# Kernel optimization log

Hardware: AMD Instinct MI355X
Metric: run time of the kernel (lower is better)

Reference implementation:

```python
import jax, jax.numpy as jnp
import numpy as np

N_NODES = 5000
N_EDGES = 40000
NUM_ATOM_TYPES = 100
HID = 32            # multiplicity of 0e and 1o in irreps_hidden
EDGE_ATTR_DIM = 8
NUM_BOND_TYPES = 5
OUT_SCALARS = 2 * 6 + 1  # max_charge=6 -> 13x0e
CUTOFF = 5.0
SQRT3 = 1.7320508075688772


def _sh(edge_vec):
    # o3.SphericalHarmonics('1x0e + 1x1o', normalize=True, normalization='component')
    d = jnp.sqrt(jnp.sum(edge_vec * edge_vec, axis=-1) + 1e-12)
    n = edge_vec / d[:, None]
    sh0 = jnp.ones(edge_vec.shape[0], edge_vec.dtype)          # [E]
    sh1 = SQRT3 * n[:, (1, 2, 0)]                              # [E,3], e3nn (y,z,x) order
    return sh0, sh1, d


def _soft_one_hot(d):
    # e3nn.math.soft_one_hot_linspace(d, 0, cutoff, 8, basis='gaussian', cutoff=True)
    values = jnp.linspace(0.0, CUTOFF, EDGE_ATTR_DIM + 2)[1:-1]
    step = CUTOFF / (EDGE_ATTR_DIM + 1)
    diff = (d[:, None] - values[None, :]) / step
    return jnp.exp(-diff * diff) / 1.12


def _mlp(x, W0, b0, W1, b1):
    # ScalarMLP(in, out, hidden=[in], SiLU)
    return jax.nn.silu(x @ W0 + b0) @ W1 + b1


def _tp_init(s, sh0, sh1, w):
    # FCTP(32x0e, 1x0e+1x1o -> 32x0e+32x1o); paths: 0e*0e->0e, 0e*1o->1o
    E = s.shape[0]
    w1 = w[:, : HID * HID].reshape(E, HID, HID)
    w2 = w[:, HID * HID :].reshape(E, HID, HID)
    c = 1.0 / np.sqrt(HID)  # fan-in = 32 per output irrep
    out_s = c * jnp.einsum('eu,euw->ew', s * sh0[:, None], w1)
    out_v = c * jnp.einsum('eu,ei,euw->ewi', s, sh1, w2)
    return out_s, out_v


def _tp_hidden(s, v, sh0, sh1, w):
    # FCTP(32x0e+32x1o, 1x0e+1x1o -> 32x0e+32x1o)
    # path order: 0e*0e->0e, 0e*1o->1o, 1o*0e->1o, 1o*1o->0e
    E = s.shape[0]
    ws = w.reshape(E, 4, HID, HID)
    c = 1.0 / np.sqrt(2 * HID)  # fan-in = 64 per output irrep
    dot = jnp.einsum('eui,ei->eu', v, sh1) / SQRT3  # CG(1,1->0) = delta/sqrt(3)
    out_s = c * (jnp.einsum('eu,euw->ew', s * sh0[:, None], ws[:, 0]) +
                 jnp.einsum('eu,euw->ew', dot, ws[:, 3]))
    out_v = c * (jnp.einsum('eu,ei,euw->ewi', s, sh1, ws[:, 1]) +
                 jnp.einsum('eui,euw->ewi', v * sh0[:, None, None], ws[:, 2]))
    return out_s, out_v


def _edge_tp(s1, v1, s2, v2, sh0, sh1, w):
    # FCTP(64x0e+64x1o (concat of two hidden), 1x0e+1x1o -> 5x0e)
    # blocks in concat order: s_src, v_src, s_dst, v_dst
    E = s1.shape[0]
    ws = w.reshape(E, 4, HID, NUM_BOND_TYPES)
    c = 1.0 / np.sqrt(4 * HID)  # fan-in = 128
    d1 = jnp.einsum('eui,ei->eu', v1, sh1) / SQRT3
    d2 = jnp.einsum('eui,ei->eu', v2, sh1) / SQRT3
    return c * (jnp.einsum('eu,euw->ew', s1 * sh0[:, None], ws[:, 0]) +
                jnp.einsum('eu,euw->ew', d1, ws[:, 1]) +
                jnp.einsum('eu,euw->ew', s2 * sh0[:, None], ws[:, 2]) +
                jnp.einsum('eu,euw->ew', d2, ws[:, 3]))


def _scatter_mean(ms, mv, dst, n):
    cnt = jax.ops.segment_sum(jnp.ones(dst.shape[0], ms.dtype), dst, num_segments=n)
    cnt = jnp.maximum(cnt, 1.0)
    s = jax.ops.segment_sum(ms, dst, num_segments=n) / cnt[:, None]
    v = jax.ops.segment_sum(mv, dst, num_segments=n) / cnt[:, None, None]
    return s, v


def setup_inputs() -> dict:
    key = jax.random.key(0)
    ks = jax.random.split(key, 16)
    def w(k, shape, fan_in):
        return jax.random.normal(k, shape, dtype=jnp.float32) / np.sqrt(fan_in)
    inp = {}
    inp['coordinates'] = jax.random.normal(ks[0], (N_NODES, 3), dtype=jnp.float32) * 1.5
    inp['atom_types'] = jax.random.randint(ks[1], (N_NODES,), 0, NUM_ATOM_TYPES)
    inp['edge_index'] = jax.random.randint(ks[2], (2, N_EDGES), 0, N_NODES)
    inp['atom_embed'] = jax.random.normal(ks[3], (NUM_ATOM_TYPES, HID), dtype=jnp.float32)
    inp['ip_W0'] = w(ks[4], (EDGE_ATTR_DIM, EDGE_ATTR_DIM), EDGE_ATTR_DIM)
    inp['ip_b0'] = jnp.zeros((EDGE_ATTR_DIM,), jnp.float32)
    inp['ip_W1'] = w(ks[5], (EDGE_ATTR_DIM, 2 * HID * HID), EDGE_ATTR_DIM)
    inp['ip_b1'] = jnp.zeros((2 * HID * HID,), jnp.float32)
    inp['ly_W0'] = w(ks[6], (EDGE_ATTR_DIM, EDGE_ATTR_DIM), EDGE_ATTR_DIM)
    inp['ly_b0'] = jnp.zeros((EDGE_ATTR_DIM,), jnp.float32)
    inp['ly_W1'] = w(ks[7], (EDGE_ATTR_DIM, 4 * HID * HID), EDGE_ATTR_DIM)
    inp['ly_b1'] = jnp.zeros((4 * HID * HID,), jnp.float32)
    inp['ly_Ws'] = jax.random.normal(ks[8], (HID, HID), dtype=jnp.float32)
    inp['ly_Wv'] = jax.random.normal(ks[9], (HID, HID), dtype=jnp.float32)
    inp['et_W0'] = w(ks[10], (EDGE_ATTR_DIM, EDGE_ATTR_DIM), EDGE_ATTR_DIM)
    inp['et_b0'] = jnp.zeros((EDGE_ATTR_DIM,), jnp.float32)
    inp['et_W1'] = w(ks[11], (EDGE_ATTR_DIM, 4 * HID * NUM_BOND_TYPES), EDGE_ATTR_DIM)
    inp['et_b1'] = jnp.zeros((4 * HID * NUM_BOND_TYPES,), jnp.float32)
    inp['no_W1'] = jax.random.normal(ks[12], (HID, OUT_SCALARS), dtype=jnp.float32)
    inp['no_W2'] = jax.random.normal(ks[13], (OUT_SCALARS, OUT_SCALARS), dtype=jnp.float32)
    return inp


def reference(coordinates, atom_types, edge_index, atom_embed,
              ip_W0, ip_b0, ip_W1, ip_b1,
              ly_W0, ly_b0, ly_W1, ly_b1, ly_Ws, ly_Wv,
              et_W0, et_b0, et_W1, et_b1, no_W1, no_W2):
    n = coordinates.shape[0]
    src, dst = edge_index[0], edge_index[1]
    edge_vec = coordinates[dst] - coordinates[src]
    sh0, sh1, d = _sh(edge_vec)
    edge_attr = _soft_one_hot(d)                              # [E,8]
    # initial projector: Conv(32x0e -> 32x0e+32x1o)
    s0 = atom_embed[atom_types]                               # [N,32]
    w_ip = _mlp(edge_attr, ip_W0, ip_b0, ip_W1, ip_b1)        # [E,2048]
    ms, mv = _tp_init(s0[src], sh0, sh1, w_ip)
    s, v = _scatter_mean(ms, mv, dst, n)                      # [N,32],[N,32,3]
    # one LinearSelfInteraction(Conv) layer
    w_ly = _mlp(edge_attr, ly_W0, ly_b0, ly_W1, ly_b1)        # [E,4096]
    ms, mv = _tp_hidden(s[src], v[src], sh0, sh1, w_ly)
    cs, cv = _scatter_mean(ms, mv, dst, n)
    lc = 1.0 / np.sqrt(HID)  # e3nn o3.Linear normalization
    s = cs + lc * (s @ ly_Ws)
    v = cv + lc * jnp.einsum('eui,uw->ewi', v, ly_Wv)
    # edge output: FCTP([h_src, h_dst], edge_sh) with radial weights
    w_et = _mlp(edge_attr, et_W0, et_b0, et_W1, et_b1)        # [E,640]
    edge_out = _edge_tp(s[src], v[src], s[dst], v[dst], sh0, sh1, w_et)  # [E,5]
    # node output MLP on detached scalar channel (13x0e)
    sd = jax.lax.stop_gradient(s)
    h = jax.nn.silu(sd @ no_W1 / np.sqrt(HID))
    node_out = h @ no_W2 / np.sqrt(OUT_SCALARS)               # [N,13]
    return edge_out, node_out
```

## Files before the change

### kernel.cpp

```cpp
#include <hip/hip_runtime.h>

#define NN 5000
#define NE 40000
#define HB 320

typedef unsigned int u32;
typedef unsigned short u16;
typedef __fp16 h16x2 __attribute__((ext_vector_type(2)));
typedef _Float16 f16x8 __attribute__((ext_vector_type(8)));
typedef __attribute__((ext_vector_type(4))) float f32x4;

union AF { u32 u[4]; f16x8 v; uint4 q; };

__device__ __forceinline__ float siluf(float x) { return x / (1.f + __expf(-x)); }

__device__ __forceinline__ u32 f2bf_u(float f) {
  u32 x = __float_as_uint(f);
  return (x + 0x7FFFu + ((x >> 16) & 1u)) >> 16;
}
__device__ __forceinline__ u16 f2bf(float f) { return (u16)f2bf_u(f); }
__device__ __forceinline__ float bf2f(u16 v) { return __uint_as_float(((u32)v) << 16); }
__device__ __forceinline__ u32 packbf2(float lo, float hi) {
  return f2bf_u(lo) | (f2bf_u(hi) << 16);
}
__device__ __forceinline__ u32 pkh2(float a, float b) {
  union { h16x2 h; u32 u; } r;
  r.h = __builtin_amdgcn_cvt_pkrtz(a, b);
  return r.u;
}
__device__ __forceinline__ u16 f2h(float v) {
  _Float16 h = (_Float16)v;
  return *(u16*)&h;
}
__device__ __forceinline__ void unpack8(uint4 q, float* f) {
  f[0] = __uint_as_float(q.x << 16); f[1] = __uint_as_float(q.x & 0xFFFF0000u);
  f[2] = __uint_as_float(q.y << 16); f[3] = __uint_as_float(q.y & 0xFFFF0000u);
  f[4] = __uint_as_float(q.z << 16); f[5] = __uint_as_float(q.z & 0xFFFF0000u);
  f[6] = __uint_as_float(q.w << 16); f[7] = __uint_as_float(q.w & 0xFFFF0000u);
}
__device__ __forceinline__ float dot8f(const float* h, const float* w, float init) {
  float a = init;
#pragma unroll
  for (int k = 0; k < 8; k++) a = fmaf(h[k], w[k], a);
  return a;
}
__device__ __forceinline__ void mlp8(const float* ea, const float* __restrict__ W0,
                                     const float* __restrict__ b0, float* h) {
#pragma unroll
  for (int j = 0; j < 8; j++) {
    float a = b0[j];
#pragma unroll
    for (int i = 0; i < 8; i++) a += ea[i] * W0[i*8 + j];
    h[j] = siluf(a);
  }
}
__device__ __forceinline__ AF mkfrag(float hs, const float* s) {
  AF a;
  a.u[0] = pkh2(hs*s[0], hs*s[1]);
  a.u[1] = pkh2(hs*s[2], hs*s[3]);
  a.u[2] = pkh2(hs*s[4], hs*s[5]);
  a.u[3] = pkh2(hs*s[6], hs*s[7]);
  return a;
}

__global__ __launch_bounds__(256) void k_conv1g(
    const float* __restrict__ coords, const int* __restrict__ eidx,
    const float* __restrict__ emb, const int* __restrict__ atype,
    const float* __restrict__ ipW0, const float* __restrict__ ipb0,
    const float* __restrict__ lyW0, const float* __restrict__ lyb0,
    const float* __restrict__ etW0, const float* __restrict__ etb0,
    const float* __restrict__ W1, const float* __restrict__ b1,
    const float* __restrict__ lyW1, const float* __restrict__ lyb1,
    float* __restrict__ sh, float* __restrict__ h_ip,
    float* __restrict__ h_ly, float* __restrict__ h_et,
    int* __restrict__ cur, int* __restrict__ perm,
    u16* __restrict__ msg, u16* __restrict__ lyT) {
  if (blockIdx.x >= HB) {
    int b = blockIdx.x - HB;
    int h = b >> 3;
    int t0 = (b & 7)*2304 + threadIdx.x*9;
#pragma unroll
    for (int j = 0; j < 9; j++) {
      int t = t0 + j;
      int kch = t >> 9, rem = t & 511;
      int col = rem >> 3, kk = rem & 7;
      int k = kch*8 + kk;
      int basec = (h == 0) ? ((col >> 5)*1024 + (col & 31))
                           : ((col < 32) ? (2048 + col) : (3072 + (col - 32)));
      float v = (k < 256) ? lyW1[(k >> 5)*4096 + basec + (k & 31)*32]
                          : lyb1[basec + (k - 256)*32];
      lyT[h*18432 + t] = f2h(v);
    }
    return;
  }
  __shared__ __align__(16) u16 B2[36*64*8];
  {
    int col = threadIdx.x & 63, pth = col >> 5, w = col & 31;
    int k0 = (threadIdx.x >> 6) * 72;
    for (int k = k0; k < k0 + 72; k++) {
      float v = (k < 256) ? W1[(k >> 5)*2048 + pth*1024 + (k & 31)*32 + w]
                          : b1[pth*1024 + (k - 256)*32 + w];
      B2[((k >> 3)*64 + col)*8 + (k & 7)] = f2h(v);
    }
  }
  if (threadIdx.x < 128) {
    int idx = threadIdx.x;
    int w = (idx >> 4) & 3, j = idx >> 6, m = idx & 15;
    int tile = blockIdx.x*4 + w + j*(HB*4);
    if (tile*16 < NE) {
      int e = tile*16 + m;
      int s = eidx[e], d = eidx[NE + e];
      float vx = coords[d*3+0] - coords[s*3+0];
      float vy = coords[d*3+1] - coords[s*3+1];
      float vz = coords[d*3+2] - coords[s*3+2];
      float dist = sqrtf(vx*vx + vy*vy + vz*vz + 1e-12f);
      float inv = 1.f / dist;
      const float SQ3 = 1.7320508075688772f;
      sh[e*3+0] = SQ3 * vy * inv;
      sh[e*3+1] = SQ3 * vz * inv;
      sh[e*3+2] = SQ3 * vx * inv;
      float ea[8];
      const float step = 5.f / 9.f;
#pragma unroll
      for (int jj = 0; jj < 8; jj++) {
        float diff = (dist - step * (float)(jj+1)) * (9.f / 5.f);
        ea[jj] = __expf(-diff*diff) * (1.f / 1.12f);
      }
      float h[8];
      mlp8(ea, ipW0, ipb0, h);
#pragma unroll
      for (int jj = 0; jj < 8; jj++) h_ip[e*8+jj] = h[jj];
      mlp8(ea, lyW0, lyb0, h);
#pragma unroll
      for (int jj = 0; jj < 8; jj++) h_ly[e*8+jj] = h[jj];
      mlp8(ea, etW0, etb0, h);
#pragma unroll
      for (int jj = 0; jj < 8; jj++) h_et[e*8+jj] = h[jj];
      int* cp = &cur[d];
      atomicCAS(cp, (int)0xAAAAAAAA, 0);
      int t = atomicAdd(cp, 1);
      if (t < 64) perm[d*64 + t] = e;
    }
  }
  __syncthreads();
  int lane = threadIdx.x & 63;
  int m = lane & 15, q = lane >> 4, wid = threadIdx.x >> 6;
  const float cs = 0.17677669529663687f;
  for (int tile = blockIdx.x*4 + wid; tile*16 < NE; tile += HB*4) {
    int e = tile*16 + m;
    int srow = atype[eidx[e]];
    float4 sA = *(const float4*)&emb[srow*32 + q*8];
    float4 sB = *(const float4*)&emb[srow*32 + q*8 + 4];
    float4 hA = *(const float4*)&h_ip[e*8];
    float4 hB = *(const float4*)&h_ip[e*8 + 4];
    float sf[8] = {sA.x,sA.y,sA.z,sA.w,sB.x,sB.y,sB.z,sB.w};
    float hf[8] = {hA.x,hA.y,hA.z,hA.w,hB.x,hB.y,hB.z,hB.w};
    f32x4 acc0 = {0.f,0.f,0.f,0.f}, acc1 = acc0, acc2 = acc0, acc3 = acc0;
#pragma unroll
    for (int ks = 0; ks < 9; ks++) {
      float hs = (ks < 8) ? hf[ks] : 1.f;
      AF a = mkfrag(hs, sf);
      int c2 = (ks*4 + q)*64;
      AF b0, b1f, b2, b3;
      b0.q  = *(const uint4*)&B2[(c2 +  0 + m)*8];
      b1f.q = *(const uint4*)&B2[(c2 + 16 + m)*8];
      b2.q  = *(const uint4*)&B2[(c2 + 32 + m)*8];
      b3.q  = *(const uint4*)&B2[(c2 + 48 + m)*8];
      acc0 = __builtin_amdgcn_mfma_f32_16x16x32_f16(a.v, b0.v,  acc0, 0, 0, 0);
      acc1 = __builtin_amdgcn_mfma_f32_16x16x32_f16(a.v, b1f.v, acc1, 0, 0, 0);
      acc2 = __builtin_amdgcn_mfma_f32_16x16x32_f16(a.v, b2.v,  acc2, 0, 0, 0);
      acc3 = __builtin_amdgcn_mfma_f32_16x16x32_f16(a.v, b3.v,  acc3, 0, 0, 0);
    }
#pragma unroll
    for (int r = 0; r < 4; r++) {
      int et = tile*16 + q*4 + r;
      u16* mp = msg + (size_t)et*128;
      mp[m]      = f2bf(cs*acc0[r]);
      mp[16 + m] = f2bf(cs*acc1[r]);
      float s0v = sh[et*3+0], s1v = sh[et*3+1], s2v = sh[et*3+2];
      float m0 = cs*acc2[r], m1 = cs*acc3[r];
      mp[32 +      m] = f2bf(m0*s0v);
      mp[64 +      m] = f2bf(m0*s1v);
      mp[96 +      m] = f2bf(m0*s2v);
      mp[32 + 16 + m] = f2bf(m1*s0v);
      mp[64 + 16 + m] = f2bf(m1*s1v);
      mp[96 + 16 + m] = f2bf(m1*s2v);
    }
  }
}

__global__ __launch_bounds__(256) void k_conv2(
    const float* __restrict__ hE, const float* __restrict__ sh,
    const float* __restrict__ s1, const float* __restrict__ v1soa,
    const int* __restrict__ eidx, const u16* __restrict__ lyT,
    u16* __restrict__ msgA, u16* __restrict__ msgB) {
  __shared__ __align__(16) u16 B2[36*64*8];
  const bool scalarHalf = blockIdx.x < HB;
  int blk = scalarHalf ? blockIdx.x : blockIdx.x - HB;
  {
    const uint4* src4 = (const uint4*)(lyT + (scalarHalf ? 0 : 18432));
    uint4* dst4 = (uint4*)B2;
    for (int t = threadIdx.x; t < 2304; t += 256) dst4[t] = src4[t];
  }
  __syncthreads();
  int lane = threadIdx.x & 63;
  int m = lane & 15, q = lane >> 4, wid = threadIdx.x >> 6;
  const float c = 0.125f;
  for (int tile = blk*4 + wid; tile*16 < NE; tile += HB*4) {
    int e = tile*16 + m;
    int srcn = eidx[e];
    float4 hA = *(const float4*)&hE[e*8];
    float4 hB = *(const float4*)&hE[e*8 + 4];
    float hf[8] = {hA.x,hA.y,hA.z,hA.w,hB.x,hB.y,hB.z,hB.w};

    if (scalarHalf) {
      float4 sA = *(const float4*)&s1[srcn*32 + q*8];
      float4 sB = *(const float4*)&s1[srcn*32 + q*8 + 4];
      float sf[8] = {sA.x,sA.y,sA.z,sA.w,sB.x,sB.y,sB.z,sB.w};
      f32x4 acc0 = {0.f,0.f,0.f,0.f}, acc1 = acc0, acc2 = acc0, acc3 = acc0;
#pragma unroll
      for (int ks = 0; ks < 9; ks++) {
        float hs = (ks < 8) ? hf[ks] : 1.f;
        AF a = mkfrag(hs, sf);
        int c2 = (ks*4 + q)*64;
        AF b0, b1f, b2, b3;
        b0.q  = *(const uint4*)&B2[(c2 +  0 + m)*8];
        b1f.q = *(const uint4*)&B2[(c2 + 16 + m)*8];
        b2.q  = *(const uint4*)&B2[(c2 + 32 + m)*8];
        b3.q  = *(const uint4*)&B2[(c2 + 48 + m)*8];
        acc0 = __builtin_amdgcn_mfma_f32_16x16x32_f16(a.v, b0.v,  acc0, 0, 0, 0);
        acc1 = __builtin_amdgcn_mfma_f32_16x16x32_f16(a.v, b1f.v, acc1, 0, 0, 0);
        acc2 = __builtin_amdgcn_mfma_f32_16x16x32_f16(a.v, b2.v,  acc2, 0, 0, 0);
        acc3 = __builtin_amdgcn_mfma_f32_16x16x32_f16(a.v, b3.v,  acc3, 0, 0, 0);
      }
#pragma unroll
      for (int r = 0; r < 4; r++) {
        int et = tile*16 + q*4 + r;
        u16* mp = msgA + (size_t)et*128;
        mp[m]      = f2bf(c*acc0[r]);
        mp[16 + m] = f2bf(c*acc1[r]);
        float s0v = sh[et*3+0], s1v = sh[et*3+1], s2v = sh[et*3+2];
        float m0 = c*acc2[r], m1 = c*acc3[r];
        mp[32 +      m] = f2bf(m0*s0v);
        mp[64 +      m] = f2bf(m0*s1v);
        mp[96 +      m] = f2bf(m0*s2v);
        mp[32 + 16 + m] = f2bf(m1*s0v);
        mp[64 + 16 + m] = f2bf(m1*s1v);
        mp[96 + 16 + m] = f2bf(m1*s2v);
      }
    } else {
      const float is3 = 0.5773502691896258f;
      float vf[3][8];
#pragma unroll
      for (int i = 0; i < 3; i++) {
        float4 aa = *(const float4*)&v1soa[i*160000 + srcn*32 + q*8];
        float4 bb = *(const float4*)&v1soa[i*160000 + srcn*32 + q*8 + 4];
        vf[i][0]=aa.x; vf[i][1]=aa.y; vf[i][2]=aa.z; vf[i][3]=aa.w;
        vf[i][4]=bb.x; vf[i][5]=bb.y; vf[i][6]=bb.z; vf[i][7]=bb.w;
      }
      float es0 = sh[e*3+0], es1 = sh[e*3+1], es2 = sh[e*3+2];
      float df[8];
#pragma unroll
      for (int j = 0; j < 8; j++)
        df[j] = (vf[0][j]*es0 + vf[1][j]*es1 + vf[2][j]*es2) * is3;
      f32x4 z = {0.f,0.f,0.f,0.f};
      f32x4 aV00 = z, aV01 = z, aV10 = z, aV11 = z, aV20 = z, aV21 = z, aD0 = z, aD1 = z;
#pragma unroll
      for (int ks = 0; ks < 9; ks++) {
        float hs = (ks < 8) ? hf[ks] : 1.f;
        int c2 = (ks*4 + q)*64;
        AF b0, b1f, b2, b3;
        b0.q  = *(const uint4*)&B2[(c2 +  0 + m)*8];
        b1f.q = *(const uint4*)&B2[(c2 + 16 + m)*8];
        b2.q  = *(const uint4*)&B2[(c2 + 32 + m)*8];
        b3.q  = *(const uint4*)&B2[(c2 + 48 + m)*8];
        AF a0 = mkfrag(hs, vf[0]);
        AF a1 = mkfrag(hs, vf[1]);
        AF a2 = mkfrag(hs, vf[2]);
        AF ad = mkfrag(hs, df);
        aV00 = __builtin_amdgcn_mfma_f32_16x16x32_f16(a0.v, b0.v,  aV00, 0, 0, 0);
        aV01 = __builtin_amdgcn_mfma_f32_16x16x32_f16(a0.v, b1f.v, aV01, 0, 0, 0);
        aV10 = __builtin_amdgcn_mfma_f32_16x16x32_f16(a1.v, b0.v,  aV10, 0, 0, 0);
        aV11 = __builtin_amdgcn_mfma_f32_16x16x32_f16(a1.v, b1f.v, aV11, 0, 0, 0);
        aV20 = __builtin_amdgcn_mfma_f32_16x16x32_f16(a2.v, b0.v,  aV20, 0, 0, 0);
        aV21 = __builtin_amdgcn_mfma_f32_16x16x32_f16(a2.v, b1f.v, aV21, 0, 0, 0);
        aD0  = __builtin_amdgcn_mfma_f32_16x16x32_f16(ad.v, b2.v,  aD0,  0, 0, 0);
        aD1  = __builtin_amdgcn_mfma_f32_16x16x32_f16(ad.v, b3.v,  aD1,  0, 0, 0);
      }
#pragma unroll
      for (int r = 0; r < 4; r++) {
        int et = tile*16 + q*4 + r;
        u16* mp = msgB + (size_t)et*128;
        mp[m]      = f2bf(c*aD0[r]);
        mp[16 + m] = f2bf(c*aD1[r]);
        mp[32 +      m] = f2bf(c*aV00[r]);
        mp[32 + 16 + m] = f2bf(c*aV01[r]);
        mp[64 +      m] = f2bf(c*aV10[r]);
        mp[64 + 16 + m] = f2bf(c*aV11[r]);
        mp[96 +      m] = f2bf(c*aV20[r]);
        mp[96 + 16 + m] = f2bf(c*aV21[r]);
      }
    }
  }
}

__global__ __launch_bounds__(256) void k_gather1(
    const u16* __restrict__ msg, const int* __restrict__ perm,
    const int* __restrict__ cur, float* __restrict__ s1,
    float* __restrict__ v1soa) {
  __shared__ int pe[2][64];
  int ln = threadIdx.x >> 7, c = threadIdx.x & 127;
  int n = blockIdx.x*2 + ln;
  int deg = min(cur[n], 64);
  if (c < 64) pe[ln][c] = perm[n*64 + c];
  __syncthreads();
  float acc = 0.f;
  for (int j = 0; j < deg; j++)
    acc += bf2f(msg[(size_t)pe[ln][j]*128 + c]);
  acc /= (float)max(deg, 1);
  if (c < 32) s1[n*32 + c] = acc;
  else { int i = (c-32) >> 5, w = (c-32) & 31; v1soa[i*160000 + n*32 + w] = acc; }
}

__global__ __launch_bounds__(256) void k_gather2(
    const u16* __restrict__ msgA, const u16* __restrict__ msgB,
    const int* __restrict__ perm, const int* __restrict__ cur,
    const float* __restrict__ s1, const float* __restrict__ v1soa,
    const float* __restrict__ Ws, const float* __restrict__ Wv,
    const float* __restrict__ noW1, const float* __restrict__ noW2,
    float* __restrict__ s2, float* __restrict__ v2, float* __restrict__ outN) {
  __shared__ int pe[2][64];
  __shared__ float sb[2][32];
  __shared__ float hb[2][13];
  int ln = threadIdx.x >> 7, c = threadIdx.x & 127;
  int n = blockIdx.x*2 + ln;
  int deg = min(cur[n], 64);
  if (c < 64) pe[ln][c] = perm[n*64 + c];
  __syncthreads();
  float acc = 0.f;
  for (int j = 0; j < deg; j++) {
    int e = pe[ln][j];
    acc += bf2f(msgA[(size_t)e*128 + c]) + bf2f(msgB[(size_t)e*128 + c]);
  }
  acc /= (float)max(deg, 1);
  const float lc = 0.17677669529663687f;
  if (c < 32) {
    float ss = 0.f;
#pragma unroll 8
    for (int u = 0; u < 32; u++) ss += s1[n*32 + u] * Ws[u*32 + c];
    float val = acc + lc*ss;
    s2[n*32 + c] = val;
    sb[ln][c] = val;
  } else {
    int i = (c-32) >> 5, w = (c-32) & 31;
    float sv = 0.f;
#pragma unroll 8
    for (int u = 0; u < 32; u++) sv += v1soa[i*160000 + n*32 + u] * Wv[u*32 + w];
    v2[n*96 + w*3 + i] = acc + lc*sv;
  }
  __syncthreads();
  const float i32 = 0.17677669529663687f;
  if (c < 13) {
    float a = 0.f;
#pragma unroll 8
    for (int u = 0; u < 32; u++) a += sb[ln][u] * noW1[u*13 + c];
    hb[ln][c] = siluf(a * i32);
  }
  __syncthreads();
  const float i13 = 0.2773500981126146f;
  if (c < 13) {
    float a = 0.f;
#pragma unroll
    for (int j = 0; j < 13; j++) a += hb[ln][j] * noW2[j*13 + c];
    outN[n*13 + c] = a * i13;
  }
}

__global__ __launch_bounds__(256) void k_e3(
    const float* __restrict__ hE, const float* __restrict__ sh,
    const float* __restrict__ s2, const float* __restrict__ v2,
    const int* __restrict__ eidx,
    const float* __restrict__ W1, const float* __restrict__ b1,
    float* __restrict__ out) {
  __shared__ uint4 WQ[640];
  __shared__ float BQ[640];
  for (int t = threadIdx.x; t < 640; t += 256) {
    int u = t & 31, pw = t >> 5, p2 = pw / 5, w = pw - p2*5;
    int col = p2*160 + u*5 + w;
    const float* s = W1 + col;
    uint4 q;
    q.x = packbf2(s[0],      s[640]);
    q.y = packbf2(s[1280],   s[1920]);
    q.z = packbf2(s[2560],   s[3200]);
    q.w = packbf2(s[3840],   s[4480]);
    WQ[t] = q;
    BQ[t] = b1[col];
  }
  __syncthreads();
  const int g = threadIdx.x >> 5, tw = threadIdx.x & 31;
  const float c = 0.08838834764831845f;
  const float is3 = 0.5773502691896258f;
  for (int p = blockIdx.x*8 + g; p*2 < NE; p += gridDim.x*8) {
    int e0 = p*2, e1 = e0 + 1;
    float h0[8], h1[8];
    {
      float4 qa = *(const float4*)&hE[e0*8];
      float4 qb = *(const float4*)&hE[e0*8+4];
      h0[0]=qa.x; h0[1]=qa.y; h0[2]=qa.z; h0[3]=qa.w;
      h0[4]=qb.x; h0[5]=qb.y; h0[6]=qb.z; h0[7]=qb.w;
      float4 qc = *(const float4*)&hE[e1*8];
      float4 qd = *(const float4*)&hE[e1*8+4];
      h1[0]=qc.x; h1[1]=qc.y; h1[2]=qc.z; h1[3]=qc.w;
      h1[4]=qd.x; h1[5]=qd.y; h1[6]=qd.z; h1[7]=qd.w;
    }
    int sA = eidx[e0], dA = eidx[NE+e0];
    int sB = eidx[e1], dB = eidx[NE+e1];
    float sa0 = sh[e0*3+0], sa1 = sh[e0*3+1], sa2 = sh[e0*3+2];
    float sb0 = sh[e1*3+0], sb1 = sh[e1*3+1], sb2 = sh[e1*3+2];
    float c00 = s2[sA*32 + tw];
    float c01 = (v2[sA*96+tw*3+0]*sa0 + v2[sA*96+tw*3+1]*sa1 + v2[sA*96+tw*3+2]*sa2) * is3;
    float c02 = s2[dA*32 + tw];
    float c03 = (v2[dA*96+tw*3+0]*sa0 + v2[dA*96+tw*3+1]*sa1 + v2[dA*96+tw*3+2]*sa2) * is3;
    float c10 = s2[sB*32 + tw];
    float c11 = (v2[sB*96+tw*3+0]*sb0 + v2[sB*96+tw*3+1]*sb1 + v2[sB*96+tw*3+2]*sb2) * is3;
    float c12 = s2[dB*32 + tw];
    float c13 = (v2[dB*96+tw*3+0]*sb0 + v2[dB*96+tw*3+1]*sb1 + v2[dB*96+tw*3+2]*sb2) * is3;
    float part0[5] = {0,0,0,0,0};
    float part1[5] = {0,0,0,0,0};
#pragma unroll
    for (int pp = 0; pp < 4; pp++) {
      float cp0 = (pp==0) ? c00 : (pp==1) ? c01 : (pp==2) ? c02 : c03;
      float cp1 = (pp==0) ? c10 : (pp==1) ? c11 : (pp==2) ? c12 : c13;
#pragma unroll
      for (int w = 0; w < 5; w++) {
        int idx = (pp*5 + w)*32 + tw;
        float f[8];
        unpack8(WQ[idx], f);
        float bv = BQ[idx];
        part0[w] = fmaf(cp0, dot8f(h0, f, bv), part0[w]);
        part1[w] = fmaf(cp1, dot8f(h1, f, bv), part1[w]);
      }
    }
#pragma unroll
    for (int off = 16; off > 0; off >>= 1)
#pragma unroll
      for (int w = 0; w < 5; w++) {
        part0[w] += __shfl_xor(part0[w], off, 32);
        part1[w] += __shfl_xor(part1[w], off, 32);
      }
    float outv = 0.f;
#pragma unroll
    for (int w = 0; w < 5; w++) {
      if (tw == w)     outv = part0[w];
      if (tw == 5 + w) outv = part1[w];
    }
    if (tw < 10) out[e0*5 + tw] = c * outv;
  }
}

extern "C" void kernel_launch(void* const* d_in, const int* in_sizes, int n_in,
                              void* d_out, int out_size, void* d_ws, size_t ws_size,
                              hipStream_t stream) {
  (void)in_sizes; (void)n_in; (void)out_size; (void)ws_size;
  const float* coords = (const float*)d_in[0];
  const int*   atype  = (const int*)d_in[1];
  const int*   eidx   = (const int*)d_in[2];
  const float* emb    = (const float*)d_in[3];
  const float* ipW0 = (const float*)d_in[4];
  const float* ipb0 = (const float*)d_in[5];
  const float* ipW1 = (const float*)d_in[6];
  const float* ipb1 = (const float*)d_in[7];
  const float* lyW0 = (const float*)d_in[8];
  const float* lyb0 = (const float*)d_in[9];
  const float* lyW1 = (const float*)d_in[10];
  const float* lyb1 = (const float*)d_in[11];
  const float* lyWs = (const float*)d_in[12];
  const float* lyWv = (const float*)d_in[13];
  const float* etW0 = (const float*)d_in[14];
  const float* etb0 = (const float*)d_in[15];
  const float* etW1 = (const float*)d_in[16];
  const float* etb1 = (const float*)d_in[17];
  const float* noW1 = (const float*)d_in[18];
  const float* noW2 = (const float*)d_in[19];

  float* ws = (float*)d_ws;
  float* sh    = ws;
  float* h_ip  = ws + 120000;
  float* h_ly  = ws + 440000;
  float* h_et  = ws + 760000;
  float* s1    = ws + 1240000;
  float* v1soa = ws + 1400000;
  float* s2    = ws + 1880000;
  float* v2    = ws + 2040000;
  int*   cur   = (int*)(ws + 2520000);
  int*   perm  = (int*)(ws + 2525000);
  u16*   msgA  = (u16*)(ws + 2845000);
  u16*   msgB  = (u16*)(ws + 5405000);
  u16*   lyT   = (u16*)(ws + 7965000);

  float* outE = (float*)d_out;
  float* outN = (float*)d_out + NE*5;

  k_conv1g<<<HB + 16, 256, 0, stream>>>(coords, eidx, emb, atype,
                                        ipW0, ipb0, lyW0, lyb0, etW0, etb0,
                                        ipW1, ipb1, lyW1, lyb1,
                                        sh, h_ip, h_ly, h_et, cur, perm, msgA, lyT);
  k_gather1<<<NN/2, 256, 0, stream>>>(msgA, perm, cur, s1, v1soa);
  k_conv2<<<2*HB, 256, 0, stream>>>(h_ly, sh, s1, v1soa, eidx, lyT, msgA, msgB);
  k_gather2<<<NN/2, 256, 0, stream>>>(msgA, msgB, perm, cur, s1, v1soa,
                                      lyWs, lyWv, noW1, noW2, s2, v2, outN);
  k_e3<<<1024, 256, 0, stream>>>(h_et, sh, s2, v2, eidx, etW1, etb1, outE);
}
```

Baseline: 170.0 us.

## Use one tile-group per block, keep per-edge data in LDS, unroll gathers

Raises the block count so each block handles exactly four 16-edge tiles (625*64 = 40000), which removes the grid-stride loops in conv1 and conv2. The per-edge radial hidden values, spherical harmonics and source atom types now stay in shared memory instead of going through the h_ip global buffer, and the h_ly/h_et stores become float4. The gather kernels unroll the neighbour sum by four to get more loads in flight, and k_e3 gets more blocks. In exchange, every block re-converts the full W1 weight tile into LDS, so that setup work is repeated across about twice as many blocks.

```diff
diff --git a/kernel.cpp b/kernel.cpp
--- a/kernel.cpp
+++ b/kernel.cpp
@@ -2,7 +2,7 @@
 
 #define NN 5000
 #define NE 40000
-#define HB 320
+#define HB 625
 
 typedef unsigned int u32;
 typedef unsigned short u16;
@@ -71,8 +71,7 @@
     const float* __restrict__ etW0, const float* __restrict__ etb0,
     const float* __restrict__ W1, const float* __restrict__ b1,
     const float* __restrict__ lyW1, const float* __restrict__ lyb1,
-    float* __restrict__ sh, float* __restrict__ h_ip,
-    float* __restrict__ h_ly, float* __restrict__ h_et,
+    float* __restrict__ sh, float* __restrict__ h_ly, float* __restrict__ h_et,
     int* __restrict__ cur, int* __restrict__ perm,
     u16* __restrict__ msg, u16* __restrict__ lyT) {
   if (blockIdx.x >= HB) {
@@ -94,6 +93,9 @@
     return;
   }
   __shared__ __align__(16) u16 B2[36*64*8];
+  __shared__ float hl[64][9];
+  __shared__ float shl[64][4];
+  __shared__ int   sAl[64];
   {
     int col = threadIdx.x & 63, pth = col >> 5, w = col & 31;
     int k0 = (threadIdx.x >> 6) * 72;
@@ -103,58 +105,60 @@
       B2[((k >> 3)*64 + col)*8 + (k & 7)] = f2h(v);
     }
   }
-  if (threadIdx.x < 128) {
+  if (threadIdx.x < 64) {
     int idx = threadIdx.x;
-    int w = (idx >> 4) & 3, j = idx >> 6, m = idx & 15;
-    int tile = blockIdx.x*4 + w + j*(HB*4);
-    if (tile*16 < NE) {
-      int e = tile*16 + m;
-      int s = eidx[e], d = eidx[NE + e];
-      float vx = coords[d*3+0] - coords[s*3+0];
-      float vy = coords[d*3+1] - coords[s*3+1];
-      float vz = coords[d*3+2] - coords[s*3+2];
-      float dist = sqrtf(vx*vx + vy*vy + vz*vz + 1e-12f);
-      float inv = 1.f / dist;
-      const float SQ3 = 1.7320508075688772f;
-      sh[e*3+0] = SQ3 * vy * inv;
-      sh[e*3+1] = SQ3 * vz * inv;
-      sh[e*3+2] = SQ3 * vx * inv;
-      float ea[8];
-      const float step = 5.f / 9.f;
-#pragma unroll
-      for (int jj = 0; jj < 8; jj++) {
-        float diff = (dist - step * (float)(jj+1)) * (9.f / 5.f);
-        ea[jj] = __expf(-diff*diff) * (1.f / 1.12f);
-      }
-      float h[8];
-      mlp8(ea, ipW0, ipb0, h);
-#pragma unroll
-      for (int jj = 0; jj < 8; jj++) h_ip[e*8+jj] = h[jj];
-      mlp8(ea, lyW0, lyb0, h);
-#pragma unroll
-      for (int jj = 0; jj < 8; jj++) h_ly[e*8+jj] = h[jj];
-      mlp8(ea, etW0, etb0, h);
-#pragma unroll
-      for (int jj = 0; jj < 8; jj++) h_et[e*8+jj] = h[jj];
-      int* cp = &cur[d];
-      atomicCAS(cp, (int)0xAAAAAAAA, 0);
-      int t = atomicAdd(cp, 1);
-      if (t < 64) perm[d*64 + t] = e;
-    }
+    int w = (idx >> 4) & 3, m = idx & 15;
+    int tile = blockIdx.x*4 + w;
+    int e = tile*16 + m;
+    int s = eidx[e], d = eidx[NE + e];
+    float vx = coords[d*3+0] - coords[s*3+0];
+    float vy = coords[d*3+1] - coords[s*3+1];
+    float vz = coords[d*3+2] - coords[s*3+2];
+    float dist = sqrtf(vx*vx + vy*vy + vz*vz + 1e-12f);
+    float inv = 1.f / dist;
+    const float SQ3 = 1.7320508075688772f;
+    float s0 = SQ3 * vy * inv;
+    float s1 = SQ3 * vz * inv;
+    float s2 = SQ3 * vx * inv;
+    sh[e*3+0] = s0; sh[e*3+1] = s1; sh[e*3+2] = s2;
+    shl[idx][0] = s0; shl[idx][1] = s1; shl[idx][2] = s2;
+    sAl[idx] = atype[s];
+    float ea[8];
+    const float step = 5.f / 9.f;
+#pragma unroll
+    for (int jj = 0; jj < 8; jj++) {
+      float diff = (dist - step * (float)(jj+1)) * (9.f / 5.f);
+      ea[jj] = __expf(-diff*diff) * (1.f / 1.12f);
+    }
+    float h[8];
+    mlp8(ea, ipW0, ipb0, h);
+#pragma unroll
+    for (int jj = 0; jj < 8; jj++) hl[idx][jj] = h[jj];
+    mlp8(ea, lyW0, lyb0, h);
+    { float4 f0 = {h[0],h[1],h[2],h[3]}, f1 = {h[4],h[5],h[6],h[7]};
+      *(float4*)&h_ly[e*8] = f0; *(float4*)&h_ly[e*8+4] = f1; }
+    mlp8(ea, etW0, etb0, h);
+    { float4 f0 = {h[0],h[1],h[2],h[3]}, f1 = {h[4],h[5],h[6],h[7]};
+      *(float4*)&h_et[e*8] = f0; *(float4*)&h_et[e*8+4] = f1; }
+    int* cp = &cur[d];
+    atomicCAS(cp, (int)0xAAAAAAAA, 0);
+    int t = atomicAdd(cp, 1);
+    if (t < 64) perm[d*64 + t] = e;
   }
   __syncthreads();
   int lane = threadIdx.x & 63;
   int m = lane & 15, q = lane >> 4, wid = threadIdx.x >> 6;
   const float cs = 0.17677669529663687f;
-  for (int tile = blockIdx.x*4 + wid; tile*16 < NE; tile += HB*4) {
-    int e = tile*16 + m;
-    int srow = atype[eidx[e]];
+  int tile = blockIdx.x*4 + wid;
+  {
+    int le = wid*16 + m;
+    int srow = sAl[le];
     float4 sA = *(const float4*)&emb[srow*32 + q*8];
     float4 sB = *(const float4*)&emb[srow*32 + q*8 + 4];
-    float4 hA = *(const float4*)&h_ip[e*8];
-    float4 hB = *(const float4*)&h_ip[e*8 + 4];
     float sf[8] = {sA.x,sA.y,sA.z,sA.w,sB.x,sB.y,sB.z,sB.w};
-    float hf[8] = {hA.x,hA.y,hA.z,hA.w,hB.x,hB.y,hB.z,hB.w};
+    float hf[8];
+#pragma unroll
+    for (int k = 0; k < 8; k++) hf[k] = hl[le][k];
     f32x4 acc0 = {0.f,0.f,0.f,0.f}, acc1 = acc0, acc2 = acc0, acc3 = acc0;
 #pragma unroll
     for (int ks = 0; ks < 9; ks++) {
@@ -173,11 +177,12 @@
     }
 #pragma unroll
     for (int r = 0; r < 4; r++) {
+      int lr = wid*16 + q*4 + r;
       int et = tile*16 + q*4 + r;
       u16* mp = msg + (size_t)et*128;
       mp[m]      = f2bf(cs*acc0[r]);
       mp[16 + m] = f2bf(cs*acc1[r]);
-      float s0v = sh[et*3+0], s1v = sh[et*3+1], s2v = sh[et*3+2];
+      float s0v = shl[lr][0], s1v = shl[lr][1], s2v = shl[lr][2];
       float m0 = cs*acc2[r], m1 = cs*acc3[r];
       mp[32 +      m] = f2bf(m0*s0v);
       mp[64 +      m] = f2bf(m0*s1v);
@@ -206,7 +211,8 @@
   int lane = threadIdx.x & 63;
   int m = lane & 15, q = lane >> 4, wid = threadIdx.x >> 6;
   const float c = 0.125f;
-  for (int tile = blk*4 + wid; tile*16 < NE; tile += HB*4) {
+  int tile = blk*4 + wid;
+  {
     int e = tile*16 + m;
     int srcn = eidx[e];
     float4 hA = *(const float4*)&hE[e*8];
@@ -315,7 +321,16 @@
   if (c < 64) pe[ln][c] = perm[n*64 + c];
   __syncthreads();
   float acc = 0.f;
-  for (int j = 0; j < deg; j++)
+  int j = 0;
+  for (; j + 4 <= deg; j += 4) {
+    int e0 = pe[ln][j], e1 = pe[ln][j+1], e2 = pe[ln][j+2], e3 = pe[ln][j+3];
+    float x0 = bf2f(msg[(size_t)e0*128 + c]);
+    float x1 = bf2f(msg[(size_t)e1*128 + c]);
+    float x2 = bf2f(msg[(size_t)e2*128 + c]);
+    float x3 = bf2f(msg[(size_t)e3*128 + c]);
+    acc += (x0 + x1) + (x2 + x3);
+  }
+  for (; j < deg; j++)
     acc += bf2f(msg[(size_t)pe[ln][j]*128 + c]);
   acc /= (float)max(deg, 1);
   if (c < 32) s1[n*32 + c] = acc;
@@ -338,7 +353,16 @@
   if (c < 64) pe[ln][c] = perm[n*64 + c];
   __syncthreads();
   float acc = 0.f;
-  for (int j = 0; j < deg; j++) {
+  int j = 0;
+  for (; j + 4 <= deg; j += 4) {
+    int e0 = pe[ln][j], e1 = pe[ln][j+1], e2 = pe[ln][j+2], e3 = pe[ln][j+3];
+    float x0 = bf2f(msgA[(size_t)e0*128 + c]) + bf2f(msgB[(size_t)e0*128 + c]);
+    float x1 = bf2f(msgA[(size_t)e1*128 + c]) + bf2f(msgB[(size_t)e1*128 + c]);
+    float x2 = bf2f(msgA[(size_t)e2*128 + c]) + bf2f(msgB[(size_t)e2*128 + c]);
+    float x3 = bf2f(msgA[(size_t)e3*128 + c]) + bf2f(msgB[(size_t)e3*128 + c]);
+    acc += (x0 + x1) + (x2 + x3);
+  }
+  for (; j < deg; j++) {
     int e = pe[ln][j];
     acc += bf2f(msgA[(size_t)e*128 + c]) + bf2f(msgB[(size_t)e*128 + c]);
   }
@@ -371,7 +395,7 @@
   if (c < 13) {
     float a = 0.f;
 #pragma unroll
-    for (int j = 0; j < 13; j++) a += hb[ln][j] * noW2[j*13 + c];
+    for (int j2 = 0; j2 < 13; j2++) a += hb[ln][j2] * noW2[j2*13 + c];
     outN[n*13 + c] = a * i13;
   }
 }
@@ -485,7 +509,6 @@
 
   float* ws = (float*)d_ws;
   float* sh    = ws;
-  float* h_ip  = ws + 120000;
   float* h_ly  = ws + 440000;
   float* h_et  = ws + 760000;
   float* s1    = ws + 1240000;
@@ -504,10 +527,10 @@
   k_conv1g<<<HB + 16, 256, 0, stream>>>(coords, eidx, emb, atype,
                                         ipW0, ipb0, lyW0, lyb0, etW0, etb0,
                                         ipW1, ipb1, lyW1, lyb1,
-                                        sh, h_ip, h_ly, h_et, cur, perm, msgA, lyT);
+                                        sh, h_ly, h_et, cur, perm, msgA, lyT);
   k_gather1<<<NN/2, 256, 0, stream>>>(msgA, perm, cur, s1, v1soa);
   k_conv2<<<2*HB, 256, 0, stream>>>(h_ly, sh, s1, v1soa, eidx, lyT, msgA, msgB);
   k_gather2<<<NN/2, 256, 0, stream>>>(msgA, msgB, perm, cur, s1, v1soa,
                                       lyWs, lyWv, noW1, noW2, s2, v2, outN);
-  k_e3<<<1024, 256, 0, stream>>>(h_et, sh, s2, v2, eidx, etW1, etb1, outE);
-}
+  k_e3<<<2500, 256, 0, stream>>>(h_et, sh, s2, v2, eidx, etW1, etb1, outE);
+}
```

Result: slower. 177.9 us (+4.6%).

## Replace CSR gather kernels with atomic scatter-add into per-node accumulators

Applied to the files above, without the earlier changes.

Each edge message is now atomically added in fp32 straight into a per-destination-node accumulator, and in-degrees are counted with a float atomic. This removes the perm/count CSR build, the two gather kernels and the bf16 per-edge message buffers. Mean normalization is deferred: the conv2 kernel scales the source-node sums by the inverse count, and a new finalize kernel applies the self-interaction and node MLP. The change adds a memset of the accumulators and many global float atomics, and the summation order becomes nondeterministic. It also drops the old 64-edge cap on node degree.

```diff
diff --git a/kernel.cpp b/kernel.cpp
--- a/kernel.cpp
+++ b/kernel.cpp
@@ -18,8 +18,6 @@
   u32 x = __float_as_uint(f);
   return (x + 0x7FFFu + ((x >> 16) & 1u)) >> 16;
 }
-__device__ __forceinline__ u16 f2bf(float f) { return (u16)f2bf_u(f); }
-__device__ __forceinline__ float bf2f(u16 v) { return __uint_as_float(((u32)v) << 16); }
 __device__ __forceinline__ u32 packbf2(float lo, float hi) {
   return f2bf_u(lo) | (f2bf_u(hi) << 16);
 }
@@ -73,8 +71,7 @@
     const float* __restrict__ lyW1, const float* __restrict__ lyb1,
     float* __restrict__ sh, float* __restrict__ h_ip,
     float* __restrict__ h_ly, float* __restrict__ h_et,
-    int* __restrict__ cur, int* __restrict__ perm,
-    u16* __restrict__ msg, u16* __restrict__ lyT) {
+    float* __restrict__ cntf, float* __restrict__ acc1, u16* __restrict__ lyT) {
   if (blockIdx.x >= HB) {
     int b = blockIdx.x - HB;
     int h = b >> 3;
@@ -106,8 +103,9 @@
   if (threadIdx.x < 128) {
     int idx = threadIdx.x;
     int w = (idx >> 4) & 3, j = idx >> 6, m = idx & 15;
-    int tile = blockIdx.x*4 + w + j*(HB*4);
-    if (tile*16 < NE) {
+    for (int it = j; ; it += 2) {
+      int tile = blockIdx.x*4 + w + it*(HB*4);
+      if (tile*16 >= NE) break;
       int e = tile*16 + m;
       int s = eidx[e], d = eidx[NE + e];
       float vx = coords[d*3+0] - coords[s*3+0];
@@ -128,18 +126,15 @@
       }
       float h[8];
       mlp8(ea, ipW0, ipb0, h);
-#pragma unroll
-      for (int jj = 0; jj < 8; jj++) h_ip[e*8+jj] = h[jj];
+      { float4 f0 = {h[0],h[1],h[2],h[3]}, f1 = {h[4],h[5],h[6],h[7]};
+        *(float4*)&h_ip[e*8] = f0; *(float4*)&h_ip[e*8+4] = f1; }
       mlp8(ea, lyW0, lyb0, h);
-#pragma unroll
-      for (int jj = 0; jj < 8; jj++) h_ly[e*8+jj] = h[jj];
+      { float4 f0 = {h[0],h[1],h[2],h[3]}, f1 = {h[4],h[5],h[6],h[7]};
+        *(float4*)&h_ly[e*8] = f0; *(float4*)&h_ly[e*8+4] = f1; }
       mlp8(ea, etW0, etb0, h);
-#pragma unroll
-      for (int jj = 0; jj < 8; jj++) h_et[e*8+jj] = h[jj];
-      int* cp = &cur[d];
-      atomicCAS(cp, (int)0xAAAAAAAA, 0);
-      int t = atomicAdd(cp, 1);
-      if (t < 64) perm[d*64 + t] = e;
+      { float4 f0 = {h[0],h[1],h[2],h[3]}, f1 = {h[4],h[5],h[6],h[7]};
+        *(float4*)&h_et[e*8] = f0; *(float4*)&h_et[e*8+4] = f1; }
+      atomicAdd(&cntf[d], 1.f);
     }
   }
   __syncthreads();
@@ -155,7 +150,7 @@
     float4 hB = *(const float4*)&h_ip[e*8 + 4];
     float sf[8] = {sA.x,sA.y,sA.z,sA.w,sB.x,sB.y,sB.z,sB.w};
     float hf[8] = {hA.x,hA.y,hA.z,hA.w,hB.x,hB.y,hB.z,hB.w};
-    f32x4 acc0 = {0.f,0.f,0.f,0.f}, acc1 = acc0, acc2 = acc0, acc3 = acc0;
+    f32x4 acc0 = {0.f,0.f,0.f,0.f}, acc1v = acc0, acc2 = acc0, acc3 = acc0;
 #pragma unroll
     for (int ks = 0; ks < 9; ks++) {
       float hs = (ks < 8) ? hf[ks] : 1.f;
@@ -166,34 +161,35 @@
       b1f.q = *(const uint4*)&B2[(c2 + 16 + m)*8];
       b2.q  = *(const uint4*)&B2[(c2 + 32 + m)*8];
       b3.q  = *(const uint4*)&B2[(c2 + 48 + m)*8];
-      acc0 = __builtin_amdgcn_mfma_f32_16x16x32_f16(a.v, b0.v,  acc0, 0, 0, 0);
-      acc1 = __builtin_amdgcn_mfma_f32_16x16x32_f16(a.v, b1f.v, acc1, 0, 0, 0);
-      acc2 = __builtin_amdgcn_mfma_f32_16x16x32_f16(a.v, b2.v,  acc2, 0, 0, 0);
-      acc3 = __builtin_amdgcn_mfma_f32_16x16x32_f16(a.v, b3.v,  acc3, 0, 0, 0);
+      acc0  = __builtin_amdgcn_mfma_f32_16x16x32_f16(a.v, b0.v,  acc0,  0, 0, 0);
+      acc1v = __builtin_amdgcn_mfma_f32_16x16x32_f16(a.v, b1f.v, acc1v, 0, 0, 0);
+      acc2  = __builtin_amdgcn_mfma_f32_16x16x32_f16(a.v, b2.v,  acc2,  0, 0, 0);
+      acc3  = __builtin_amdgcn_mfma_f32_16x16x32_f16(a.v, b3.v,  acc3,  0, 0, 0);
     }
 #pragma unroll
     for (int r = 0; r < 4; r++) {
       int et = tile*16 + q*4 + r;
-      u16* mp = msg + (size_t)et*128;
-      mp[m]      = f2bf(cs*acc0[r]);
-      mp[16 + m] = f2bf(cs*acc1[r]);
+      int dn = eidx[NE + et];
+      float* ap = acc1 + (size_t)dn*128;
       float s0v = sh[et*3+0], s1v = sh[et*3+1], s2v = sh[et*3+2];
+      atomicAdd(&ap[m],       cs*acc0[r]);
+      atomicAdd(&ap[16 + m],  cs*acc1v[r]);
       float m0 = cs*acc2[r], m1 = cs*acc3[r];
-      mp[32 +      m] = f2bf(m0*s0v);
-      mp[64 +      m] = f2bf(m0*s1v);
-      mp[96 +      m] = f2bf(m0*s2v);
-      mp[32 + 16 + m] = f2bf(m1*s0v);
-      mp[64 + 16 + m] = f2bf(m1*s1v);
-      mp[96 + 16 + m] = f2bf(m1*s2v);
+      atomicAdd(&ap[32 + m],  m0*s0v);
+      atomicAdd(&ap[64 + m],  m0*s1v);
+      atomicAdd(&ap[96 + m],  m0*s2v);
+      atomicAdd(&ap[48 + m],  m1*s0v);
+      atomicAdd(&ap[80 + m],  m1*s1v);
+      atomicAdd(&ap[112 + m], m1*s2v);
     }
   }
 }
 
 __global__ __launch_bounds__(256) void k_conv2(
     const float* __restrict__ hE, const float* __restrict__ sh,
-    const float* __restrict__ s1, const float* __restrict__ v1soa,
+    const float* __restrict__ acc1, const float* __restrict__ cntf,
     const int* __restrict__ eidx, const u16* __restrict__ lyT,
-    u16* __restrict__ msgA, u16* __restrict__ msgB) {
+    float* __restrict__ acc2out) {
   __shared__ __align__(16) u16 B2[36*64*8];
   const bool scalarHalf = blockIdx.x < HB;
   int blk = scalarHalf ? blockIdx.x : blockIdx.x - HB;
@@ -209,15 +205,17 @@
   for (int tile = blk*4 + wid; tile*16 < NE; tile += HB*4) {
     int e = tile*16 + m;
     int srcn = eidx[e];
+    float inv = 1.f / fmaxf(cntf[srcn], 1.f);
     float4 hA = *(const float4*)&hE[e*8];
     float4 hB = *(const float4*)&hE[e*8 + 4];
     float hf[8] = {hA.x,hA.y,hA.z,hA.w,hB.x,hB.y,hB.z,hB.w};
 
     if (scalarHalf) {
-      float4 sA = *(const float4*)&s1[srcn*32 + q*8];
-      float4 sB = *(const float4*)&s1[srcn*32 + q*8 + 4];
-      float sf[8] = {sA.x,sA.y,sA.z,sA.w,sB.x,sB.y,sB.z,sB.w};
-      f32x4 acc0 = {0.f,0.f,0.f,0.f}, acc1 = acc0, acc2 = acc0, acc3 = acc0;
+      float4 sA = *(const float4*)&acc1[(size_t)srcn*128 + q*8];
+      float4 sB = *(const float4*)&acc1[(size_t)srcn*128 + q*8 + 4];
+      float sf[8] = {inv*sA.x,inv*sA.y,inv*sA.z,inv*sA.w,
+                     inv*sB.x,inv*sB.y,inv*sB.z,inv*sB.w};
+      f32x4 acc0 = {0.f,0.f,0.f,0.f}, acc1v = acc0, acc2 = acc0, acc3 = acc0;
 #pragma unroll
       for (int ks = 0; ks < 9; ks++) {
         float hs = (ks < 8) ? hf[ks] : 1.f;
@@ -228,35 +226,36 @@
         b1f.q = *(const uint4*)&B2[(c2 + 16 + m)*8];
         b2.q  = *(const uint4*)&B2[(c2 + 32 + m)*8];
         b3.q  = *(const uint4*)&B2[(c2 + 48 + m)*8];
-        acc0 = __builtin_amdgcn_mfma_f32_16x16x32_f16(a.v, b0.v,  acc0, 0, 0, 0);
-        acc1 = __builtin_amdgcn_mfma_f32_16x16x32_f16(a.v, b1f.v, acc1, 0, 0, 0);
-        acc2 = __builtin_amdgcn_mfma_f32_16x16x32_f16(a.v, b2.v,  acc2, 0, 0, 0);
-        acc3 = __builtin_amdgcn_mfma_f32_16x16x32_f16(a.v, b3.v,  acc3, 0, 0, 0);
+        acc0  = __builtin_amdgcn_mfma_f32_16x16x32_f16(a.v, b0.v,  acc0,  0, 0, 0);
+        acc1v = __builtin_amdgcn_mfma_f32_16x16x32_f16(a.v, b1f.v, acc1v, 0, 0, 0);
+        acc2  = __builtin_amdgcn_mfma_f32_16x16x32_f16(a.v, b2.v,  acc2,  0, 0, 0);
+        acc3  = __builtin_amdgcn_mfma_f32_16x16x32_f16(a.v, b3.v,  acc3,  0, 0, 0);
       }
 #pragma unroll
       for (int r = 0; r < 4; r++) {
         int et = tile*16 + q*4 + r;
-        u16* mp = msgA + (size_t)et*128;
-        mp[m]      = f2bf(c*acc0[r]);
-        mp[16 + m] = f2bf(c*acc1[r]);
+        int dn = eidx[NE + et];
+        float* ap = acc2out + (size_t)dn*128;
         float s0v = sh[et*3+0], s1v = sh[et*3+1], s2v = sh[et*3+2];
+        atomicAdd(&ap[m],       c*acc0[r]);
+        atomicAdd(&ap[16 + m],  c*acc1v[r]);
         float m0 = c*acc2[r], m1 = c*acc3[r];
-        mp[32 +      m] = f2bf(m0*s0v);
-        mp[64 +      m] = f2bf(m0*s1v);
-        mp[96 +      m] = f2bf(m0*s2v);
-        mp[32 + 16 + m] = f2bf(m1*s0v);
-        mp[64 + 16 + m] = f2bf(m1*s1v);
-        mp[96 + 16 + m] = f2bf(m1*s2v);
+        atomicAdd(&ap[32 + m],  m0*s0v);
+        atomicAdd(&ap[64 + m],  m0*s1v);
+        atomicAdd(&ap[96 + m],  m0*s2v);
+        atomicAdd(&ap[48 + m],  m1*s0v);
+        atomicAdd(&ap[80 + m],  m1*s1v);
+        atomicAdd(&ap[112 + m], m1*s2v);
       }
     } else {
       const float is3 = 0.5773502691896258f;
       float vf[3][8];
 #pragma unroll
       for (int i = 0; i < 3; i++) {
-        float4 aa = *(const float4*)&v1soa[i*160000 + srcn*32 + q*8];
-        float4 bb = *(const float4*)&v1soa[i*160000 + srcn*32 + q*8 + 4];
-        vf[i][0]=aa.x; vf[i][1]=aa.y; vf[i][2]=aa.z; vf[i][3]=aa.w;
-        vf[i][4]=bb.x; vf[i][5]=bb.y; vf[i][6]=bb.z; vf[i][7]=bb.w;
+        float4 aa = *(const float4*)&acc1[(size_t)srcn*128 + 32 + i*32 + q*8];
+        float4 bb = *(const float4*)&acc1[(size_t)srcn*128 + 32 + i*32 + q*8 + 4];
+        vf[i][0]=inv*aa.x; vf[i][1]=inv*aa.y; vf[i][2]=inv*aa.z; vf[i][3]=inv*aa.w;
+        vf[i][4]=inv*bb.x; vf[i][5]=inv*bb.y; vf[i][6]=inv*bb.z; vf[i][7]=inv*bb.w;
       }
       float es0 = sh[e*3+0], es1 = sh[e*3+1], es2 = sh[e*3+2];
       float df[8];
@@ -290,89 +289,63 @@
 #pragma unroll
       for (int r = 0; r < 4; r++) {
         int et = tile*16 + q*4 + r;
-        u16* mp = msgB + (size_t)et*128;
-        mp[m]      = f2bf(c*aD0[r]);
-        mp[16 + m] = f2bf(c*aD1[r]);
-        mp[32 +      m] = f2bf(c*aV00[r]);
-        mp[32 + 16 + m] = f2bf(c*aV01[r]);
-        mp[64 +      m] = f2bf(c*aV10[r]);
-        mp[64 + 16 + m] = f2bf(c*aV11[r]);
-        mp[96 +      m] = f2bf(c*aV20[r]);
-        mp[96 + 16 + m] = f2bf(c*aV21[r]);
-      }
-    }
-  }
-}
-
-__global__ __launch_bounds__(256) void k_gather1(
-    const u16* __restrict__ msg, const int* __restrict__ perm,
-    const int* __restrict__ cur, float* __restrict__ s1,
-    float* __restrict__ v1soa) {
-  __shared__ int pe[2][64];
-  int ln = threadIdx.x >> 7, c = threadIdx.x & 127;
-  int n = blockIdx.x*2 + ln;
-  int deg = min(cur[n], 64);
-  if (c < 64) pe[ln][c] = perm[n*64 + c];
-  __syncthreads();
-  float acc = 0.f;
-  for (int j = 0; j < deg; j++)
-    acc += bf2f(msg[(size_t)pe[ln][j]*128 + c]);
-  acc /= (float)max(deg, 1);
-  if (c < 32) s1[n*32 + c] = acc;
-  else { int i = (c-32) >> 5, w = (c-32) & 31; v1soa[i*160000 + n*32 + w] = acc; }
-}
-
-__global__ __launch_bounds__(256) void k_gather2(
-    const u16* __restrict__ msgA, const u16* __restrict__ msgB,
-    const int* __restrict__ perm, const int* __restrict__ cur,
-    const float* __restrict__ s1, const float* __restrict__ v1soa,
+        int dn = eidx[NE + et];
+        float* ap = acc2out + (size_t)dn*128;
+        atomicAdd(&ap[m],       c*aD0[r]);
+        atomicAdd(&ap[16 + m],  c*aD1[r]);
+        atomicAdd(&ap[32 + m],  c*aV00[r]);
+        atomicAdd(&ap[48 + m],  c*aV01[r]);
+        atomicAdd(&ap[64 + m],  c*aV10[r]);
+        atomicAdd(&ap[80 + m],  c*aV11[r]);
+        atomicAdd(&ap[96 + m],  c*aV20[r]);
+        atomicAdd(&ap[112 + m], c*aV21[r]);
+      }
+    }
+  }
+}
+
+__global__ __launch_bounds__(256) void k_fin(
+    const float* __restrict__ acc1, const float* __restrict__ acc2,
+    const float* __restrict__ cntf,
     const float* __restrict__ Ws, const float* __restrict__ Wv,
     const float* __restrict__ noW1, const float* __restrict__ noW2,
     float* __restrict__ s2, float* __restrict__ v2, float* __restrict__ outN) {
-  __shared__ int pe[2][64];
   __shared__ float sb[2][32];
   __shared__ float hb[2][13];
   int ln = threadIdx.x >> 7, c = threadIdx.x & 127;
   int n = blockIdx.x*2 + ln;
-  int deg = min(cur[n], 64);
-  if (c < 64) pe[ln][c] = perm[n*64 + c];
-  __syncthreads();
-  float acc = 0.f;
-  for (int j = 0; j < deg; j++) {
-    int e = pe[ln][j];
-    acc += bf2f(msgA[(size_t)e*128 + c]) + bf2f(msgB[(size_t)e*128 + c]);
-  }
-  acc /= (float)max(deg, 1);
+  float inv = 1.f / fmaxf(cntf[n], 1.f);
+  float a = acc2[(size_t)n*128 + c];
   const float lc = 0.17677669529663687f;
   if (c < 32) {
     float ss = 0.f;
 #pragma unroll 8
-    for (int u = 0; u < 32; u++) ss += s1[n*32 + u] * Ws[u*32 + c];
-    float val = acc + lc*ss;
+    for (int u = 0; u < 32; u++) ss += acc1[(size_t)n*128 + u] * Ws[u*32 + c];
+    float val = inv * (a + lc*ss);
     s2[n*32 + c] = val;
     sb[ln][c] = val;
   } else {
     int i = (c-32) >> 5, w = (c-32) & 31;
     float sv = 0.f;
 #pragma unroll 8
-    for (int u = 0; u < 32; u++) sv += v1soa[i*160000 + n*32 + u] * Wv[u*32 + w];
-    v2[n*96 + w*3 + i] = acc + lc*sv;
+    for (int u = 0; u < 32; u++) sv += acc1[(size_t)n*128 + 32 + i*32 + u] * Wv[u*32 + w];
+    v2[n*96 + w*3 + i] = inv * (a + lc*sv);
   }
   __syncthreads();
   const float i32 = 0.17677669529663687f;
   if (c < 13) {
-    float a = 0.f;
+    float aa = 0.f;
 #pragma unroll 8
-    for (int u = 0; u < 32; u++) a += sb[ln][u] * noW1[u*13 + c];
-    hb[ln][c] = siluf(a * i32);
+    for (int u = 0; u < 32; u++) aa += sb[ln][u] * noW1[u*13 + c];
+    hb[ln][c] = siluf(aa * i32);
   }
   __syncthreads();
   const float i13 = 0.2773500981126146f;
   if (c < 13) {
-    float a = 0.f;
-#pragma unroll
-    for (int j = 0; j < 13; j++) a += hb[ln][j] * noW2[j*13 + c];
-    outN[n*13 + c] = a * i13;
+    float aa = 0.f;
+#pragma unroll
+    for (int j2 = 0; j2 < 13; j2++) aa += hb[ln][j2] * noW2[j2*13 + c];
+    outN[n*13 + c] = aa * i13;
   }
 }
 
@@ -488,26 +461,24 @@
   float* h_ip  = ws + 120000;
   float* h_ly  = ws + 440000;
   float* h_et  = ws + 760000;
-  float* s1    = ws + 1240000;
-  float* v1soa = ws + 1400000;
-  float* s2    = ws + 1880000;
-  float* v2    = ws + 2040000;
-  int*   cur   = (int*)(ws + 2520000);
-  int*   perm  = (int*)(ws + 2525000);
-  u16*   msgA  = (u16*)(ws + 2845000);
-  u16*   msgB  = (u16*)(ws + 5405000);
-  u16*   lyT   = (u16*)(ws + 7965000);
+  float* s2    = ws + 1080000;
+  float* v2    = ws + 1240000;
+  float* acc1  = ws + 1720000;
+  float* acc2  = ws + 2360000;
+  float* cntf  = ws + 3000000;
+  u16*   lyT   = (u16*)(ws + 3005000);
 
   float* outE = (float*)d_out;
   float* outN = (float*)d_out + NE*5;
+
+  hipMemsetAsync(ws + 1720000, 0, (size_t)(3005000 - 1720000) * sizeof(float), stream);
 
   k_conv1g<<<HB + 16, 256, 0, stream>>>(coords, eidx, emb, atype,
                                         ipW0, ipb0, lyW0, lyb0, etW0, etb0,
                                         ipW1, ipb1, lyW1, lyb1,
-                                        sh, h_ip, h_ly, h_et, cur, perm, msgA, lyT);
-  k_gather1<<<NN/2, 256, 0, stream>>>(msgA, perm, cur, s1, v1soa);
-  k_conv2<<<2*HB, 256, 0, stream>>>(h_ly, sh, s1, v1soa, eidx, lyT, msgA, msgB);
-  k_gather2<<<NN/2, 256, 0, stream>>>(msgA, msgB, perm, cur, s1, v1soa,
-                                      lyWs, lyWv, noW1, noW2, s2, v2, outN);
+                                        sh, h_ip, h_ly, h_et, cntf, acc1, lyT);
+  k_conv2<<<2*HB, 256, 0, stream>>>(h_ly, sh, acc1, cntf, eidx, lyT, acc2);
+  k_fin<<<NN/2, 256, 0, stream>>>(acc1, acc2, cntf, lyWs, lyWv, noW1, noW2,
+                                  s2, v2, outN);
   k_e3<<<1024, 256, 0, stream>>>(h_et, sh, s2, v2, eidx, etW1, etb1, outE);
 }
```

Result: slower. 196.9 us (+15.8%).
